# Performance work log

Measured on AMD Instinct MI355X. Metric: run time of the kernel, lower is better.

Reference implementation:

```python
import jax, jax.numpy as jnp
import numpy as np

L, D, H, HD, FF, V, NH, S = 5, 1024, 8, 128, 4096, 2048, 15, 2
EPS = 1e-6
THETA = 10000.0


def rms_norm(x, w):
    x32 = x.astype(jnp.float32)
    y = x32 * jax.lax.rsqrt(jnp.mean(x32 * x32, axis=-1, keepdims=True) + EPS)
    return (y * w.astype(jnp.float32)).astype(x.dtype)


def rotate_half(x):
    x1, x2 = x[..., : HD // 2], x[..., HD // 2:]
    return jnp.concatenate((-x2, x1), axis=-1)


def setup_inputs() -> dict:
    key = jax.random.key(0)
    ks = jax.random.split(key, 20)
    s = 0.02
    inp = {
        "past_hidden": jax.random.normal(ks[0], (1, 1, D), jnp.float32),
        "cb0_token": jax.random.randint(ks[1], (1, 1), 0, V, jnp.int32),
        "codec_emb": jax.random.normal(ks[2], (V, D), jnp.float32) * s,
        "Wq": jax.random.normal(ks[3], (L, D, H * HD), jnp.float32) * s,
        "Wk": jax.random.normal(ks[4], (L, D, H * HD), jnp.float32) * s,
        "Wv": jax.random.normal(ks[5], (L, D, H * HD), jnp.float32) * s,
        "Wo": jax.random.normal(ks[6], (L, H * HD, D), jnp.float32) * s,
        "q_norm_w": jnp.ones((L, HD), jnp.float32),
        "k_norm_w": jnp.ones((L, HD), jnp.float32),
        "ln1_w": jnp.ones((L, D), jnp.float32),
        "ln2_w": jnp.ones((L, D), jnp.float32),
        "Wgate": jax.random.normal(ks[7], (L, D, FF), jnp.float32) * s,
        "Wup": jax.random.normal(ks[8], (L, D, FF), jnp.float32) * s,
        "Wdown": jax.random.normal(ks[9], (L, FF, D), jnp.float32) * s,
        "final_norm_w": jnp.ones((D,), jnp.float32),
        "lm_heads": jax.random.normal(ks[10], (NH, D, V), jnp.float32) * s,
    }
    return inp


def reference(past_hidden, codec_emb, Wq, Wk, Wv, Wo, q_norm_w, k_norm_w,
              ln1_w, ln2_w, Wgate, Wup, Wdown, final_norm_w, lm_heads,
              cb0_token):
    # Embed CB0 token and build 2-token prefill sequence [1, 2, D].
    cb0_embed = codec_emb[cb0_token]            # [1, 1, D]
    h = jnp.concatenate([past_hidden, cb0_embed], axis=1)

    # Rotary cos/sin for positions [0, 1]: [1, 1, S, HD].
    pos = jnp.arange(S, dtype=jnp.float32)
    inv_freq = 1.0 / (THETA ** (jnp.arange(0, HD, 2, dtype=jnp.float32) / HD))
    freqs = pos[:, None] * inv_freq[None, :]    # [S, HD/2]
    emb = jnp.concatenate([freqs, freqs], axis=-1)
    cos = jnp.cos(emb)[None, None]
    sin = jnp.sin(emb)[None, None]

    causal_mask = jnp.array([[0.0, -1e9], [0.0, 0.0]], jnp.float32)
    scale = 1.0 / np.sqrt(HD)

    def layer_step(h, p):
        wq, wk, wv, wo, qn, kn, l1, l2, wg, wu, wd = p
        res = h
        x = rms_norm(h, l1)                     # [1, S, D]
        q = (x @ wq).reshape(1, S, H, HD)
        k = (x @ wk).reshape(1, S, H, HD)
        v = (x @ wv).reshape(1, S, H, HD)
        q = rms_norm(q, qn)                     # per-head qk-norm
        k = rms_norm(k, kn)
        q = q.transpose(0, 2, 1, 3)             # [1, H, S, HD]
        k = k.transpose(0, 2, 1, 3)
        v = v.transpose(0, 2, 1, 3)
        q = q * cos + rotate_half(q) * sin
        k = k * cos + rotate_half(k) * sin
        attn = jnp.einsum('bhqd,bhkd->bhqk', q, k) * scale + causal_mask
        w = jax.nn.softmax(attn.astype(jnp.float32), axis=-1).astype(q.dtype)
        o = jnp.einsum('bhqk,bhkd->bhqd', w, v)
        o = o.transpose(0, 2, 1, 3).reshape(1, S, H * HD) @ wo
        h = res + o
        res = h
        x = rms_norm(h, l2)
        mlp = (jax.nn.silu(x @ wg) * (x @ wu)) @ wd
        return res + mlp, (k, v)

    h, (ks_, vs_) = jax.lax.scan(
        layer_step, h,
        (Wq, Wk, Wv, Wo, q_norm_w, k_norm_w, ln1_w, ln2_w, Wgate, Wup, Wdown))

    h = rms_norm(h, final_norm_w)
    last = h[:, -1, :]                          # [1, D]
    all_logits = jnp.einsum('bd,ndv->nbv', last, lm_heads)  # [15, 1, V]
    # Interleave keys/values per layer: [2L, 1, H, S, HD].
    kv_cache = jnp.stack([ks_, vs_], axis=1).reshape(2 * L, 1, H, S, HD)
    return all_logits, kv_cache
```

## Files before the change

kernel.cpp:

```cpp
#include <hip/hip_runtime.h>
#include <math.h>

#define EPS 1e-6f


__global__ void init_kernel(const float* __restrict__ past_hidden,
                            const float* __restrict__ codec_emb,
                            const int* __restrict__ tok,
                            float* __restrict__ ws,
                            float* __restrict__ logits)
{
    size_t idx = (size_t)blockIdx.x * blockDim.x + threadIdx.x;
    size_t stride = (size_t)gridDim.x * blockDim.x;
    for (size_t i = idx; i < 30720; i += stride) ws[2048 + i] = 0.f;
    for (size_t i = idx; i < 81920; i += stride) ws[43008 + i] = 0.f;
    for (size_t i = idx; i < 30720; i += stride) logits[i] = 0.f;
    int t = tok[0];
    for (size_t i = idx; i < 1024; i += stride) {
        ws[i]        = past_hidden[i];
        ws[1024 + i] = codec_emb[(size_t)t * 1024 + i];
    }
}

template <int S>
__global__ __launch_bounds__(256) void gemv_rms(
    const float* __restrict__ hbuf,
    const float* __restrict__ nw,
    const float* __restrict__ W0,
    const float* __restrict__ W1,
    const float* __restrict__ W2,
    size_t w_zstride,
    float* __restrict__ out,
    int out_sstride, int out_zstride,
    int D, int N)
{
    __shared__ float xs[S * 1024];
    __shared__ float red[S * 1024];
    __shared__ float tot[S];
    const int t = threadIdx.x;

    const float* W;
    if (W1) W = (blockIdx.z == 0) ? W0 : ((blockIdx.z == 1) ? W1 : W2);
    else    W = W0 + (size_t)blockIdx.z * w_zstride;
    float* outz = out + (size_t)blockIdx.z * out_zstride;

    if (nw) {
        float ss[S];
#pragma unroll
        for (int s = 0; s < S; ++s) ss[s] = 0.f;
        for (int dd = t; dd < D; dd += 256) {
#pragma unroll
            for (int s = 0; s < S; ++s) {
                float v = hbuf[s * D + dd];
                xs[s * 1024 + dd] = v;
                ss[s] += v * v;
            }
        }
#pragma unroll
        for (int s = 0; s < S; ++s) {
            red[t] = ss[s]; __syncthreads();
            for (int off = 128; off >= 1; off >>= 1) {
                if (t < off) red[t] += red[t + off];
                __syncthreads();
            }
            if (t == 0) tot[s] = red[0];
            __syncthreads();
        }
        float sc[S];
#pragma unroll
        for (int s = 0; s < S; ++s) sc[s] = rsqrtf(tot[s] / (float)D + EPS);
        for (int dd = t; dd < D; dd += 256) {
            float wv = nw[dd];
#pragma unroll
            for (int s = 0; s < S; ++s)
                xs[s * 1024 + dd] = xs[s * 1024 + dd] * sc[s] * wv;
        }
        __syncthreads();
    } else {
        for (int dd = t; dd < D; dd += 256) {
#pragma unroll
            for (int s = 0; s < S; ++s) xs[s * 1024 + dd] = hbuf[s * D + dd];
        }
        __syncthreads();
    }

    const int lane = t & 63;
    const int dp = t >> 6;
    const int j = blockIdx.x * 256 + lane * 4;
    const int d0 = blockIdx.y * 64 + dp * 16;

    float acc[S][4];
#pragma unroll
    for (int s = 0; s < S; ++s) { acc[s][0] = acc[s][1] = acc[s][2] = acc[s][3] = 0.f; }
#pragma unroll
    for (int i = 0; i < 16; ++i) {
        int dd = d0 + i;
        float4 w4 = *reinterpret_cast<const float4*>(W + (size_t)dd * N + j);
#pragma unroll
        for (int s = 0; s < S; ++s) {
            float xv = xs[s * 1024 + dd];
            acc[s][0] += xv * w4.x; acc[s][1] += xv * w4.y;
            acc[s][2] += xv * w4.z; acc[s][3] += xv * w4.w;
        }
    }
    __syncthreads();
#pragma unroll
    for (int s = 0; s < S; ++s)
#pragma unroll
        for (int c = 0; c < 4; ++c)
            red[(dp * S + s) * 256 + lane * 4 + c] = acc[s][c];
    __syncthreads();
    for (int o = t; o < S * 256; o += 256) {
        int s = o >> 8;
        int col = o & 255;
        float sum = 0.f;
#pragma unroll
        for (int dp2 = 0; dp2 < 4; ++dp2) sum += red[(dp2 * S + s) * 256 + col];
        atomicAdd(outz + (size_t)s * out_sstride + blockIdx.x * 256 + col, sum);
    }
}

__global__ void attn_kernel(const float* __restrict__ qkv,
                            const float* __restrict__ qnw,
                            const float* __restrict__ knw,
                            float* __restrict__ ao,
                            float* __restrict__ kvc)
{
    const int h = blockIdx.x;
    const int d = threadIdx.x;
    __shared__ float rbuf[128];
    __shared__ float qb[2][128], kb[2][128];

    float q[2], k[2], v[2];
#pragma unroll
    for (int s = 0; s < 2; ++s) {
        q[s] = qkv[s * 3072 +        h * 128 + d];
        k[s] = qkv[s * 3072 + 1024 + h * 128 + d];
        v[s] = qkv[s * 3072 + 2048 + h * 128 + d];
    }
    auto bred = [&](float val) -> float {
        rbuf[d] = val; __syncthreads();
        for (int off = 64; off >= 1; off >>= 1) {
            if (d < off) rbuf[d] += rbuf[d + off];
            __syncthreads();
        }
        float r = rbuf[0]; __syncthreads();
        return r;
    };
    float qs0 = bred(q[0] * q[0]);
    float qs1 = bred(q[1] * q[1]);
    float ks0 = bred(k[0] * k[0]);
    float ks1 = bred(k[1] * k[1]);
    float qsc[2] = { rsqrtf(qs0 / 128.f + EPS), rsqrtf(qs1 / 128.f + EPS) };
    float ksc[2] = { rsqrtf(ks0 / 128.f + EPS), rsqrtf(ks1 / 128.f + EPS) };
#pragma unroll
    for (int s = 0; s < 2; ++s) {
        qb[s][d] = q[s] * qsc[s] * qnw[d];
        kb[s][d] = k[s] * ksc[s] * knw[d];
    }
    __syncthreads();
    float invf = powf(10000.f, -(float)(d & 63) / 64.f);
    float qr[2], kr[2];
#pragma unroll
    for (int s = 0; s < 2; ++s) {
        float ang = (float)s * invf;
        float c = cosf(ang), si = sinf(ang);
        float qrot = (d < 64) ? -qb[s][d + 64] : qb[s][d - 64];
        float krot = (d < 64) ? -kb[s][d + 64] : kb[s][d - 64];
        qr[s] = qb[s][d] * c + qrot * si;
        kr[s] = kb[s][d] * c + krot * si;
    }
#pragma unroll
    for (int s = 0; s < 2; ++s) {
        kvc[h * 256 + s * 128 + d]        = kr[s];
        kvc[2048 + h * 256 + s * 128 + d] = v[s];
    }
    float p00 = bred(qr[0] * kr[0]);
    float p01 = bred(qr[0] * kr[1]);
    float p10 = bred(qr[1] * kr[0]);
    float p11 = bred(qr[1] * kr[1]);
    const float scale = 0.08838834764831845f;
    float s00 = p00 * scale, s01 = p01 * scale - 1e9f;
    float m0 = fmaxf(s00, s01);
    float e0 = expf(s00 - m0), e1 = expf(s01 - m0);
    float in0 = 1.f / (e0 + e1);
    float w00 = e0 * in0, w01 = e1 * in0;
    float s10 = p10 * scale, s11 = p11 * scale;
    float m1 = fmaxf(s10, s11);
    float f0 = expf(s10 - m1), f1 = expf(s11 - m1);
    float in1 = 1.f / (f0 + f1);
    float w10 = f0 * in1, w11 = f1 * in1;

    ao[0 * 1024 + h * 128 + d] = w00 * v[0] + w01 * v[1];
    ao[1 * 1024 + h * 128 + d] = w10 * v[0] + w11 * v[1];
}

__global__ __launch_bounds__(256) void gemv_down(
    const float* __restrict__ gu,
    const float* __restrict__ W,
    float* __restrict__ out)
{
    __shared__ float a[2][64];
    __shared__ float red[2048];
    const int t = threadIdx.x;
    const int d0 = blockIdx.y * 64;
    if (t < 128) {
        int s = t >> 6, f = d0 + (t & 63);
        float g = gu[s * 8192 + f];
        float u = gu[s * 8192 + 4096 + f];
        float sg = g / (1.f + expf(-g));
        a[s][t & 63] = sg * u;
    }
    __syncthreads();
    const int lane = t & 63;
    const int dp = t >> 6;
    const int j = blockIdx.x * 256 + lane * 4;
    float acc[2][4] = {{0.f,0.f,0.f,0.f},{0.f,0.f,0.f,0.f}};
#pragma unroll
    for (int i = 0; i < 16; ++i) {
        int dl = dp * 16 + i;
        int dd = d0 + dl;
        float4 w4 = *reinterpret_cast<const float4*>(W + (size_t)dd * 1024 + j);
#pragma unroll
        for (int s = 0; s < 2; ++s) {
            float xv = a[s][dl];
            acc[s][0] += xv * w4.x; acc[s][1] += xv * w4.y;
            acc[s][2] += xv * w4.z; acc[s][3] += xv * w4.w;
        }
    }
#pragma unroll
    for (int s = 0; s < 2; ++s)
#pragma unroll
        for (int c = 0; c < 4; ++c)
            red[(dp * 2 + s) * 256 + lane * 4 + c] = acc[s][c];
    __syncthreads();
    for (int o = t; o < 512; o += 256) {
        int s = o >> 8, col = o & 255;
        float sum = 0.f;
#pragma unroll
        for (int dp2 = 0; dp2 < 4; ++dp2) sum += red[(dp2 * 2 + s) * 256 + col];
        atomicAdd(out + s * 1024 + blockIdx.x * 256 + col, sum);
    }
}

__global__ void final_norm_kernel(const float* __restrict__ h,
                                  const float* __restrict__ w,
                                  float* __restrict__ outx)
{
    __shared__ float rbuf[256];
    __shared__ float tot;
    int t = threadIdx.x;
    float ss = 0.f;
    for (int dd = t; dd < 1024; dd += 256) { float v = h[1024 + dd]; ss += v * v; }
    rbuf[t] = ss; __syncthreads();
    for (int off = 128; off >= 1; off >>= 1) {
        if (t < off) rbuf[t] += rbuf[t + off];
        __syncthreads();
    }
    if (t == 0) tot = rbuf[0];
    __syncthreads();
    float sc = rsqrtf(tot / 1024.f + EPS);
    for (int dd = t; dd < 1024; dd += 256) outx[dd] = h[1024 + dd] * sc * w[dd];
}

extern "C" void kernel_launch(void* const* d_in, const int* in_sizes, int n_in,
                              void* d_out, int out_size, void* d_ws, size_t ws_size,
                              hipStream_t stream)
{
    const float* past_hidden = (const float*)d_in[0];
    const int*   cb0         = (const int*)d_in[1];
    const float* codec_emb   = (const float*)d_in[2];
    const float* Wq  = (const float*)d_in[3];
    const float* Wk  = (const float*)d_in[4];
    const float* Wv  = (const float*)d_in[5];
    const float* Wo  = (const float*)d_in[6];
    const float* qnw = (const float*)d_in[7];
    const float* knw = (const float*)d_in[8];
    const float* ln1 = (const float*)d_in[9];
    const float* ln2 = (const float*)d_in[10];
    const float* Wg  = (const float*)d_in[11];
    const float* Wu  = (const float*)d_in[12];
    const float* Wd  = (const float*)d_in[13];
    const float* fnw = (const float*)d_in[14];
    const float* lmh = (const float*)d_in[15];

    float* out = (float*)d_out;
    float* ws  = (float*)d_ws;
    float* h      = ws;
    float* qkvb   = ws + 2048;
    float* aob    = ws + 32768;
    float* gub    = ws + 43008;
    float* lastn  = ws + 124928;
    float* logits = out;
    float* kvc    = out + 30720;

    init_kernel<<<256, 256, 0, stream>>>(past_hidden, codec_emb, cb0, ws, logits);

    for (int l = 0; l < 5; ++l) {
        const float* wq = Wq + (size_t)l * 1024 * 1024;
        const float* wk = Wk + (size_t)l * 1024 * 1024;
        const float* wv = Wv + (size_t)l * 1024 * 1024;
        const float* wo = Wo + (size_t)l * 1024 * 1024;
        const float* wg = Wg + (size_t)l * 1024 * 4096;
        const float* wu = Wu + (size_t)l * 1024 * 4096;
        const float* wd = Wd + (size_t)l * 4096 * 1024;
        float* qkv = qkvb + (size_t)l * 6144;
        float* ao  = aob  + (size_t)l * 2048;
        float* gu  = gub  + (size_t)l * 16384;

        gemv_rms<2><<<dim3(4, 16, 3), 256, 0, stream>>>(
            h, ln1 + l * 1024, wq, wk, wv, 0, qkv, 3072, 1024, 1024, 1024);
        attn_kernel<<<8, 128, 0, stream>>>(qkv, qnw + l * 128, knw + l * 128, ao,
                                           kvc + (size_t)(2 * l) * 2048);
        gemv_rms<2><<<dim3(4, 16, 1), 256, 0, stream>>>(
            ao, nullptr, wo, nullptr, nullptr, 0, h, 1024, 0, 1024, 1024);
        gemv_rms<2><<<dim3(16, 16, 2), 256, 0, stream>>>(
            h, ln2 + l * 1024, wg, wu, wu, 0, gu, 8192, 4096, 1024, 4096);
        gemv_down<<<dim3(4, 64), 256, 0, stream>>>(gu, wd, h);
    }

    final_norm_kernel<<<1, 256, 0, stream>>>(h, fnw, lastn);
    gemv_rms<1><<<dim3(8, 16, 15), 256, 0, stream>>>(
        lastn, nullptr, lmh, nullptr, nullptr, (size_t)1024 * 2048,
        logits, 2048, 2048, 1024, 2048);
}
```

Measured before the change: 539.7 us.

## Fuse attention into O-projection, fold RMS norms into GEMVs, prefetch weights to registers

Attention is merged into the O-projection GEMV: every block recomputes per-head qk-norm, RoPE and softmax with wave shuffles, then multiplies by its Wo tile. This drops the separate attention launch and the ao round trip. The RMS-norm scale in gemv_rms is now applied after accumulation using a shuffle reduction, so weight loads are issued into registers before the norm. The final norm kernel is folded into the lm_head GEMV. Grids are doubled with fewer rows per block to get more memory parallelism, at the cost of redundant attention work in every block and more atomics.

```diff
diff --git a/kernel.cpp b/kernel.cpp
--- a/kernel.cpp
+++ b/kernel.cpp
@@ -3,6 +3,12 @@
 
 #define EPS 1e-6f
 
+
+__device__ __forceinline__ float red32(float v) {
+#pragma unroll
+    for (int m = 16; m >= 1; m >>= 1) v += __shfl_xor(v, m, 64);
+    return v;
+}
 
 __global__ void init_kernel(const float* __restrict__ past_hidden,
                             const float* __restrict__ codec_emb,
@@ -22,7 +28,7 @@
     }
 }
 
-template <int S>
+template <int S, int R>
 __global__ __launch_bounds__(256) void gemv_rms(
     const float* __restrict__ hbuf,
     const float* __restrict__ nw,
@@ -31,154 +37,157 @@
     const float* __restrict__ W2,
     size_t w_zstride,
     float* __restrict__ out,
-    int out_sstride, int out_zstride,
-    int D, int N)
+    int out_sstride, int out_zstride, int N)
 {
     __shared__ float xs[S * 1024];
-    __shared__ float red[S * 1024];
-    __shared__ float tot[S];
+    __shared__ float sstot[S * 4];
     const int t = threadIdx.x;
+    const int lane = t & 63;
+    const int dp = t >> 6;
 
     const float* W;
     if (W1) W = (blockIdx.z == 0) ? W0 : ((blockIdx.z == 1) ? W1 : W2);
     else    W = W0 + (size_t)blockIdx.z * w_zstride;
     float* outz = out + (size_t)blockIdx.z * out_zstride;
 
-    if (nw) {
-        float ss[S];
-#pragma unroll
-        for (int s = 0; s < S; ++s) ss[s] = 0.f;
-        for (int dd = t; dd < D; dd += 256) {
-#pragma unroll
-            for (int s = 0; s < S; ++s) {
-                float v = hbuf[s * D + dd];
-                xs[s * 1024 + dd] = v;
-                ss[s] += v * v;
-            }
-        }
+    const int j = blockIdx.x * 256 + lane * 4;
+    const int d0 = blockIdx.y * (4 * R) + dp * R;
+
+    float4 wreg[R];
+    const float* Wp = W + (size_t)d0 * N + j;
+#pragma unroll
+    for (int i = 0; i < R; ++i)
+        wreg[i] = *reinterpret_cast<const float4*>(Wp + (size_t)i * N);
+
+    float ss[S];
+    {
+        float4 nw4 = *reinterpret_cast<const float4*>(nw + t * 4);
 #pragma unroll
         for (int s = 0; s < S; ++s) {
-            red[t] = ss[s]; __syncthreads();
-            for (int off = 128; off >= 1; off >>= 1) {
-                if (t < off) red[t] += red[t + off];
-                __syncthreads();
-            }
-            if (t == 0) tot[s] = red[0];
-            __syncthreads();
-        }
-        float sc[S];
-#pragma unroll
-        for (int s = 0; s < S; ++s) sc[s] = rsqrtf(tot[s] / (float)D + EPS);
-        for (int dd = t; dd < D; dd += 256) {
-            float wv = nw[dd];
-#pragma unroll
-            for (int s = 0; s < S; ++s)
-                xs[s * 1024 + dd] = xs[s * 1024 + dd] * sc[s] * wv;
-        }
-        __syncthreads();
-    } else {
-        for (int dd = t; dd < D; dd += 256) {
-#pragma unroll
-            for (int s = 0; s < S; ++s) xs[s * 1024 + dd] = hbuf[s * D + dd];
-        }
-        __syncthreads();
-    }
-
-    const int lane = t & 63;
-    const int dp = t >> 6;
-    const int j = blockIdx.x * 256 + lane * 4;
-    const int d0 = blockIdx.y * 64 + dp * 16;
+            float4 xv = *reinterpret_cast<const float4*>(hbuf + s * 1024 + t * 4);
+            ss[s] = xv.x * xv.x + xv.y * xv.y + xv.z * xv.z + xv.w * xv.w;
+            float4 xw = make_float4(xv.x * nw4.x, xv.y * nw4.y, xv.z * nw4.z, xv.w * nw4.w);
+            *reinterpret_cast<float4*>(&xs[s * 1024 + t * 4]) = xw;
+        }
+    }
+    __syncthreads();
 
     float acc[S][4];
 #pragma unroll
     for (int s = 0; s < S; ++s) { acc[s][0] = acc[s][1] = acc[s][2] = acc[s][3] = 0.f; }
 #pragma unroll
-    for (int i = 0; i < 16; ++i) {
+    for (int i = 0; i < R; ++i) {
         int dd = d0 + i;
-        float4 w4 = *reinterpret_cast<const float4*>(W + (size_t)dd * N + j);
 #pragma unroll
         for (int s = 0; s < S; ++s) {
             float xv = xs[s * 1024 + dd];
-            acc[s][0] += xv * w4.x; acc[s][1] += xv * w4.y;
-            acc[s][2] += xv * w4.z; acc[s][3] += xv * w4.w;
-        }
-    }
-    __syncthreads();
+            acc[s][0] += xv * wreg[i].x; acc[s][1] += xv * wreg[i].y;
+            acc[s][2] += xv * wreg[i].z; acc[s][3] += xv * wreg[i].w;
+        }
+    }
+
+#pragma unroll
+    for (int s = 0; s < S; ++s) {
+        float v = ss[s];
+#pragma unroll
+        for (int m = 32; m >= 1; m >>= 1) v += __shfl_xor(v, m, 64);
+        if (lane == 0) sstot[s * 4 + dp] = v;
+    }
+    __syncthreads();
+    float sc[S];
+#pragma unroll
+    for (int s = 0; s < S; ++s) {
+        float tot = sstot[s * 4 + 0] + sstot[s * 4 + 1] + sstot[s * 4 + 2] + sstot[s * 4 + 3];
+        sc[s] = rsqrtf(tot / 1024.f + EPS);
+    }
+
 #pragma unroll
     for (int s = 0; s < S; ++s)
 #pragma unroll
         for (int c = 0; c < 4; ++c)
-            red[(dp * S + s) * 256 + lane * 4 + c] = acc[s][c];
+            xs[(dp * S + s) * 256 + lane * 4 + c] = acc[s][c] * sc[s];
     __syncthreads();
     for (int o = t; o < S * 256; o += 256) {
         int s = o >> 8;
         int col = o & 255;
         float sum = 0.f;
 #pragma unroll
-        for (int dp2 = 0; dp2 < 4; ++dp2) sum += red[(dp2 * S + s) * 256 + col];
+        for (int p = 0; p < 4; ++p) sum += xs[(p * S + s) * 256 + col];
         atomicAdd(outz + (size_t)s * out_sstride + blockIdx.x * 256 + col, sum);
     }
 }
 
-__global__ void attn_kernel(const float* __restrict__ qkv,
-                            const float* __restrict__ qnw,
-                            const float* __restrict__ knw,
-                            float* __restrict__ ao,
-                            float* __restrict__ kvc)
-{
-    const int h = blockIdx.x;
-    const int d = threadIdx.x;
-    __shared__ float rbuf[128];
-    __shared__ float qb[2][128], kb[2][128];
-
-    float q[2], k[2], v[2];
+__global__ __launch_bounds__(256) void attn_o_kernel(
+    const float* __restrict__ qkv,
+    const float* __restrict__ qnw,
+    const float* __restrict__ knw,
+    const float* __restrict__ W,
+    float* __restrict__ out,
+    float* __restrict__ kvc)
+{
+    __shared__ float xs[2048];
+    const int t = threadIdx.x;
+    const int lane = t & 63;
+    const int dp = t >> 6;
+    const int j = blockIdx.x * 256 + lane * 4;
+    const int d0 = blockIdx.y * 16 + dp * 4;
+
+    float4 wreg[4];
+    const float* Wp = W + (size_t)d0 * 1024 + j;
+#pragma unroll
+    for (int i = 0; i < 4; ++i)
+        wreg[i] = *reinterpret_cast<const float4*>(Wp + (size_t)i * 1024);
+
+    const int hh = t >> 5;
+    const int g = t & 31;
+    float q[2][4], k[2][4], v[2][4];
+#pragma unroll
+    for (int s = 0; s < 2; ++s)
+#pragma unroll
+        for (int c = 0; c < 4; ++c) {
+            int d = g + c * 32;
+            q[s][c] = qkv[s * 3072 +        hh * 128 + d];
+            k[s][c] = qkv[s * 3072 + 1024 + hh * 128 + d];
+            v[s][c] = qkv[s * 3072 + 2048 + hh * 128 + d];
+        }
 #pragma unroll
     for (int s = 0; s < 2; ++s) {
-        q[s] = qkv[s * 3072 +        h * 128 + d];
-        k[s] = qkv[s * 3072 + 1024 + h * 128 + d];
-        v[s] = qkv[s * 3072 + 2048 + h * 128 + d];
-    }
-    auto bred = [&](float val) -> float {
-        rbuf[d] = val; __syncthreads();
-        for (int off = 64; off >= 1; off >>= 1) {
-            if (d < off) rbuf[d] += rbuf[d + off];
-            __syncthreads();
-        }
-        float r = rbuf[0]; __syncthreads();
-        return r;
-    };
-    float qs0 = bred(q[0] * q[0]);
-    float qs1 = bred(q[1] * q[1]);
-    float ks0 = bred(k[0] * k[0]);
-    float ks1 = bred(k[1] * k[1]);
-    float qsc[2] = { rsqrtf(qs0 / 128.f + EPS), rsqrtf(qs1 / 128.f + EPS) };
-    float ksc[2] = { rsqrtf(ks0 / 128.f + EPS), rsqrtf(ks1 / 128.f + EPS) };
-#pragma unroll
-    for (int s = 0; s < 2; ++s) {
-        qb[s][d] = q[s] * qsc[s] * qnw[d];
-        kb[s][d] = k[s] * ksc[s] * knw[d];
-    }
-    __syncthreads();
-    float invf = powf(10000.f, -(float)(d & 63) / 64.f);
-    float qr[2], kr[2];
-#pragma unroll
-    for (int s = 0; s < 2; ++s) {
-        float ang = (float)s * invf;
-        float c = cosf(ang), si = sinf(ang);
-        float qrot = (d < 64) ? -qb[s][d + 64] : qb[s][d - 64];
-        float krot = (d < 64) ? -kb[s][d + 64] : kb[s][d - 64];
-        qr[s] = qb[s][d] * c + qrot * si;
-        kr[s] = kb[s][d] * c + krot * si;
-    }
-#pragma unroll
-    for (int s = 0; s < 2; ++s) {
-        kvc[h * 256 + s * 128 + d]        = kr[s];
-        kvc[2048 + h * 256 + s * 128 + d] = v[s];
-    }
-    float p00 = bred(qr[0] * kr[0]);
-    float p01 = bred(qr[0] * kr[1]);
-    float p10 = bred(qr[1] * kr[0]);
-    float p11 = bred(qr[1] * kr[1]);
+        float sq = q[s][0]*q[s][0] + q[s][1]*q[s][1] + q[s][2]*q[s][2] + q[s][3]*q[s][3];
+        float sk = k[s][0]*k[s][0] + k[s][1]*k[s][1] + k[s][2]*k[s][2] + k[s][3]*k[s][3];
+        sq = red32(sq); sk = red32(sk);
+        float qsc = rsqrtf(sq / 128.f + EPS);
+        float ksc = rsqrtf(sk / 128.f + EPS);
+#pragma unroll
+        for (int c = 0; c < 4; ++c) {
+            q[s][c] *= qsc * qnw[g + c * 32];
+            k[s][c] *= ksc * knw[g + c * 32];
+        }
+    }
+    float inv0 = powf(10000.f, -(float)g / 64.f);
+    float inv1 = powf(10000.f, -(float)(g + 32) / 64.f);
+    float cA = cosf(inv0), sA = sinf(inv0);
+    float cB = cosf(inv1), sB = sinf(inv1);
+    float q1[4] = { q[1][0]*cA - q[1][2]*sA, q[1][1]*cB - q[1][3]*sB,
+                    q[1][2]*cA + q[1][0]*sA, q[1][3]*cB + q[1][1]*sB };
+    float k1[4] = { k[1][0]*cA - k[1][2]*sA, k[1][1]*cB - k[1][3]*sB,
+                    k[1][2]*cA + k[1][0]*sA, k[1][3]*cB + k[1][1]*sB };
+
+    if (blockIdx.x == 0 && blockIdx.y == 0) {
+#pragma unroll
+        for (int c = 0; c < 4; ++c) {
+            int d = g + c * 32;
+            kvc[hh * 256 +       d] = k[0][c];
+            kvc[hh * 256 + 128 + d] = k1[c];
+            kvc[2048 + hh * 256 +       d] = v[0][c];
+            kvc[2048 + hh * 256 + 128 + d] = v[1][c];
+        }
+    }
+
+    float p00 = red32(q[0][0]*k[0][0] + q[0][1]*k[0][1] + q[0][2]*k[0][2] + q[0][3]*k[0][3]);
+    float p01 = red32(q[0][0]*k1[0]   + q[0][1]*k1[1]   + q[0][2]*k1[2]   + q[0][3]*k1[3]);
+    float p10 = red32(q1[0]*k[0][0]   + q1[1]*k[0][1]   + q1[2]*k[0][2]   + q1[3]*k[0][3]);
+    float p11 = red32(q1[0]*k1[0]     + q1[1]*k1[1]     + q1[2]*k1[2]     + q1[3]*k1[3]);
+
     const float scale = 0.08838834764831845f;
     float s00 = p00 * scale, s01 = p01 * scale - 1e9f;
     float m0 = fmaxf(s00, s01);
@@ -191,8 +200,39 @@
     float in1 = 1.f / (f0 + f1);
     float w10 = f0 * in1, w11 = f1 * in1;
 
-    ao[0 * 1024 + h * 128 + d] = w00 * v[0] + w01 * v[1];
-    ao[1 * 1024 + h * 128 + d] = w10 * v[0] + w11 * v[1];
+#pragma unroll
+    for (int c = 0; c < 4; ++c) {
+        int d = g + c * 32;
+        xs[       hh * 128 + d] = w00 * v[0][c] + w01 * v[1][c];
+        xs[1024 + hh * 128 + d] = w10 * v[0][c] + w11 * v[1][c];
+    }
+    __syncthreads();
+
+    float acc[2][4] = {{0.f,0.f,0.f,0.f},{0.f,0.f,0.f,0.f}};
+#pragma unroll
+    for (int i = 0; i < 4; ++i) {
+        int dd = d0 + i;
+#pragma unroll
+        for (int s = 0; s < 2; ++s) {
+            float xv = xs[s * 1024 + dd];
+            acc[s][0] += xv * wreg[i].x; acc[s][1] += xv * wreg[i].y;
+            acc[s][2] += xv * wreg[i].z; acc[s][3] += xv * wreg[i].w;
+        }
+    }
+    __syncthreads();
+#pragma unroll
+    for (int s = 0; s < 2; ++s)
+#pragma unroll
+        for (int c = 0; c < 4; ++c)
+            xs[(dp * 2 + s) * 256 + lane * 4 + c] = acc[s][c];
+    __syncthreads();
+    for (int o = t; o < 512; o += 256) {
+        int s = o >> 8, col = o & 255;
+        float sum = 0.f;
+#pragma unroll
+        for (int p = 0; p < 4; ++p) sum += xs[(p * 2 + s) * 256 + col];
+        atomicAdd(out + (size_t)s * 1024 + blockIdx.x * 256 + col, sum);
+    }
 }
 
 __global__ __launch_bounds__(256) void gemv_down(
@@ -200,32 +240,38 @@
     const float* __restrict__ W,
     float* __restrict__ out)
 {
-    __shared__ float a[2][64];
+    __shared__ float a[2][32];
     __shared__ float red[2048];
     const int t = threadIdx.x;
-    const int d0 = blockIdx.y * 64;
-    if (t < 128) {
-        int s = t >> 6, f = d0 + (t & 63);
-        float g = gu[s * 8192 + f];
-        float u = gu[s * 8192 + 4096 + f];
-        float sg = g / (1.f + expf(-g));
-        a[s][t & 63] = sg * u;
-    }
-    __syncthreads();
     const int lane = t & 63;
     const int dp = t >> 6;
     const int j = blockIdx.x * 256 + lane * 4;
+    const int f0 = blockIdx.y * 32 + dp * 8;
+
+    float4 wreg[8];
+    const float* Wp = W + (size_t)f0 * 1024 + j;
+#pragma unroll
+    for (int i = 0; i < 8; ++i)
+        wreg[i] = *reinterpret_cast<const float4*>(Wp + (size_t)i * 1024);
+
+    if (t < 64) {
+        int s = t >> 5, x = t & 31;
+        int f = blockIdx.y * 32 + x;
+        float g = gu[s * 8192 + f];
+        float u = gu[s * 8192 + 4096 + f];
+        a[s][x] = g / (1.f + expf(-g)) * u;
+    }
+    __syncthreads();
+
     float acc[2][4] = {{0.f,0.f,0.f,0.f},{0.f,0.f,0.f,0.f}};
 #pragma unroll
-    for (int i = 0; i < 16; ++i) {
-        int dl = dp * 16 + i;
-        int dd = d0 + dl;
-        float4 w4 = *reinterpret_cast<const float4*>(W + (size_t)dd * 1024 + j);
+    for (int i = 0; i < 8; ++i) {
+        int dl = dp * 8 + i;
 #pragma unroll
         for (int s = 0; s < 2; ++s) {
             float xv = a[s][dl];
-            acc[s][0] += xv * w4.x; acc[s][1] += xv * w4.y;
-            acc[s][2] += xv * w4.z; acc[s][3] += xv * w4.w;
+            acc[s][0] += xv * wreg[i].x; acc[s][1] += xv * wreg[i].y;
+            acc[s][2] += xv * wreg[i].z; acc[s][3] += xv * wreg[i].w;
         }
     }
 #pragma unroll
@@ -238,29 +284,9 @@
         int s = o >> 8, col = o & 255;
         float sum = 0.f;
 #pragma unroll
-        for (int dp2 = 0; dp2 < 4; ++dp2) sum += red[(dp2 * 2 + s) * 256 + col];
-        atomicAdd(out + s * 1024 + blockIdx.x * 256 + col, sum);
-    }
-}
-
-__global__ void final_norm_kernel(const float* __restrict__ h,
-                                  const float* __restrict__ w,
-                                  float* __restrict__ outx)
-{
-    __shared__ float rbuf[256];
-    __shared__ float tot;
-    int t = threadIdx.x;
-    float ss = 0.f;
-    for (int dd = t; dd < 1024; dd += 256) { float v = h[1024 + dd]; ss += v * v; }
-    rbuf[t] = ss; __syncthreads();
-    for (int off = 128; off >= 1; off >>= 1) {
-        if (t < off) rbuf[t] += rbuf[t + off];
-        __syncthreads();
-    }
-    if (t == 0) tot = rbuf[0];
-    __syncthreads();
-    float sc = rsqrtf(tot / 1024.f + EPS);
-    for (int dd = t; dd < 1024; dd += 256) outx[dd] = h[1024 + dd] * sc * w[dd];
+        for (int p = 0; p < 4; ++p) sum += red[(p * 2 + s) * 256 + col];
+        atomicAdd(out + (size_t)s * 1024 + blockIdx.x * 256 + col, sum);
+    }
 }
 
 extern "C" void kernel_launch(void* const* d_in, const int* in_sizes, int n_in,
@@ -288,9 +314,7 @@
     float* ws  = (float*)d_ws;
     float* h      = ws;
     float* qkvb   = ws + 2048;
-    float* aob    = ws + 32768;
     float* gub    = ws + 43008;
-    float* lastn  = ws + 124928;
     float* logits = out;
     float* kvc    = out + 30720;
 
@@ -305,22 +329,18 @@
         const float* wu = Wu + (size_t)l * 1024 * 4096;
         const float* wd = Wd + (size_t)l * 4096 * 1024;
         float* qkv = qkvb + (size_t)l * 6144;
-        float* ao  = aob  + (size_t)l * 2048;
         float* gu  = gub  + (size_t)l * 16384;
 
-        gemv_rms<2><<<dim3(4, 16, 3), 256, 0, stream>>>(
-            h, ln1 + l * 1024, wq, wk, wv, 0, qkv, 3072, 1024, 1024, 1024);
-        attn_kernel<<<8, 128, 0, stream>>>(qkv, qnw + l * 128, knw + l * 128, ao,
-                                           kvc + (size_t)(2 * l) * 2048);
-        gemv_rms<2><<<dim3(4, 16, 1), 256, 0, stream>>>(
-            ao, nullptr, wo, nullptr, nullptr, 0, h, 1024, 0, 1024, 1024);
-        gemv_rms<2><<<dim3(16, 16, 2), 256, 0, stream>>>(
-            h, ln2 + l * 1024, wg, wu, wu, 0, gu, 8192, 4096, 1024, 4096);
-        gemv_down<<<dim3(4, 64), 256, 0, stream>>>(gu, wd, h);
-    }
-
-    final_norm_kernel<<<1, 256, 0, stream>>>(h, fnw, lastn);
-    gemv_rms<1><<<dim3(8, 16, 15), 256, 0, stream>>>(
-        lastn, nullptr, lmh, nullptr, nullptr, (size_t)1024 * 2048,
-        logits, 2048, 2048, 1024, 2048);
-}
+        gemv_rms<2, 8><<<dim3(4, 32, 3), 256, 0, stream>>>(
+            h, ln1 + l * 1024, wq, wk, wv, 0, qkv, 3072, 1024, 1024);
+        attn_o_kernel<<<dim3(4, 64), 256, 0, stream>>>(
+            qkv, qnw + l * 128, knw + l * 128, wo, h, kvc + (size_t)(2 * l) * 2048);
+        gemv_rms<2, 8><<<dim3(16, 32, 2), 256, 0, stream>>>(
+            h, ln2 + l * 1024, wg, wu, wu, 0, gu, 8192, 4096, 4096);
+        gemv_down<<<dim3(4, 128), 256, 0, stream>>>(gu, wd, h);
+    }
+
+    gemv_rms<1, 16><<<dim3(8, 16, 15), 256, 0, stream>>>(
+        h + 1024, fnw, lmh, nullptr, nullptr, (size_t)1024 * 2048,
+        logits, 2048, 2048, 2048);
+}
```

Result: faster. 470.0 us (-12.9%).
